# Performance work log

Measured on AMD Instinct MI355X. Metric: run time of the kernel, lower is better.

The kernel has to match this reference:

```python
import jax, jax.numpy as jnp
import numpy as np

NUM_GROUPS = 8
EPS = 1e-5
QB = 128.0  # 2 ** (8 - 1), b = 8 activation bits


def setup_inputs() -> dict:
    key = jax.random.key(0)
    k1, k2, k3 = jax.random.split(key, 3)
    B, IN, OUT = 8192, 4096, 4096
    x = jax.random.normal(k1, (B, IN), jnp.float32)
    # emulates the int8 sign buffer (values in {-1, +1}) stored as float
    qw = jnp.sign(jax.random.normal(k2, (OUT, IN), jnp.float32))
    bias = jax.random.normal(k3, (OUT,), jnp.float32) * 0.02
    return {"x": x, "qw": qw, "bias": bias}


def _ste_sign(z):
    # straight-through estimator: sign in fwd, identity grad in bwd
    return jax.lax.stop_gradient(jnp.sign(z) - z) + z


def reference(x, qw, bias):
    g = NUM_GROUPS
    # dequantize_weights: global mean-abs scale over the sign buffer
    alpha = jnp.mean(jnp.abs(qw))
    w = qw * alpha                                  # [OUT, IN]
    OUT, IN = w.shape
    # binarize_weights_groupwise: groups along out_features rows
    wg = w.reshape(g, OUT // g, IN)
    alpha_g = jnp.mean(jnp.abs(wg), axis=(1, 2), keepdims=True)
    bw = _ste_sign(wg - alpha_g).reshape(OUT, IN)   # values in {-1, 0, +1}
    # linear
    out = x @ bw.T + bias                           # [B, OUT]
    # quantize_activations_groupwise: groups along batch dim, b=8
    B = out.shape[0]
    og = out.reshape(g, B // g, OUT)
    gamma_g = jnp.max(jnp.abs(og), axis=(1, 2), keepdims=True)
    q = jnp.clip(og * QB / (gamma_g + EPS), -QB + EPS, QB - EPS)
    return q.reshape(B, OUT)
```

## Files before the change

### kernel.cpp

```cpp
#include <hip/hip_runtime.h>
#include <hip/hip_bf16.h>
#include <stdint.h>

#define B_DIM   8192
#define IN_DIM  4096
#define OUT_DIM 4096
#define QB_V    128.0f
#define EPS_V   1e-5f

typedef __attribute__((ext_vector_type(4))) float  f32x4;
typedef __attribute__((ext_vector_type(8))) __bf16 bf16x8;
typedef __attribute__((ext_vector_type(4))) __bf16 bf16x4;

__device__ __forceinline__ void gload_lds16(const void* g, void* l) {
  void* gp = const_cast<void*>(g);
  __builtin_amdgcn_global_load_lds(
      (__attribute__((address_space(1))) void*)gp,
      (__attribute__((address_space(3))) void*)l, 16, 0, 0);
}

__device__ __forceinline__ __bf16 sgnb(float d) {
  return (__bf16)((d > 0.f) ? 1.f : (d < 0.f ? -1.f : 0.f));
}

__global__ void k_init(unsigned* ws) {
  int t = threadIdx.x;
  if (t < 16) ws[t] = 0u;
}

__global__ __launch_bounds__(256) void k_qw_sums(const float* __restrict__ qw,
                                                 float* __restrict__ sums) {
  __shared__ float red[4];
  const int t = threadIdx.x;
  const size_t base = (size_t)blockIdx.x * 4096;
  float s = 0.f;
#pragma unroll
  for (int j = 0; j < 4; ++j) {
    f32x4 v = *(const f32x4*)(qw + base + (size_t)j * 1024 + t * 4);
    s += fabsf(v.x) + fabsf(v.y) + fabsf(v.z) + fabsf(v.w);
  }
#pragma unroll
  for (int off = 32; off > 0; off >>= 1) s += __shfl_xor(s, off);
  if ((t & 63) == 0) red[t >> 6] = s;
  __syncthreads();
  if (t == 0) {
    float bs = red[0] + red[1] + red[2] + red[3];
    atomicAdd(sums + (blockIdx.x >> 9), bs);
  }
}

__global__ __launch_bounds__(256) void k_conv_bw(const float* __restrict__ qw,
                                                 const float* __restrict__ sums,
                                                 __bf16* __restrict__ bw) {
  const size_t i = ((size_t)blockIdx.x * 256 + threadIdx.x) * 16;
  const int g = (int)(i >> 21);
  const float mu = sums[g] * (1.0f / 2097152.0f);
#pragma unroll
  for (int h = 0; h < 2; ++h) {
    f32x4 v0 = *(const f32x4*)(qw + i + h * 8);
    f32x4 v1 = *(const f32x4*)(qw + i + h * 8 + 4);
    bf16x8 r;
    r[0] = sgnb(v0.x - mu); r[1] = sgnb(v0.y - mu);
    r[2] = sgnb(v0.z - mu); r[3] = sgnb(v0.w - mu);
    r[4] = sgnb(v1.x - mu); r[5] = sgnb(v1.y - mu);
    r[6] = sgnb(v1.z - mu); r[7] = sgnb(v1.w - mu);
    *(bf16x8*)(bw + i + h * 8) = r;
  }
}

__global__ __launch_bounds__(256) void k_conv_x(const float* __restrict__ x,
                                                __bf16* __restrict__ xb) {
  const size_t i = ((size_t)blockIdx.x * 256 + threadIdx.x) * 16;
#pragma unroll
  for (int h = 0; h < 2; ++h) {
    f32x4 v0 = *(const f32x4*)(x + i + h * 8);
    f32x4 v1 = *(const f32x4*)(x + i + h * 8 + 4);
    bf16x8 r;
    r[0] = (__bf16)v0.x; r[1] = (__bf16)v0.y;
    r[2] = (__bf16)v0.z; r[3] = (__bf16)v0.w;
    r[4] = (__bf16)v1.x; r[5] = (__bf16)v1.y;
    r[6] = (__bf16)v1.z; r[7] = (__bf16)v1.w;
    *(bf16x8*)(xb + i + h * 8) = r;
  }
}

template <int AMODE>
__global__ __launch_bounds__(256) void k_gemm(
    const __bf16* __restrict__ xa, const float* __restrict__ xf,
    const __bf16* __restrict__ bwb, const float* __restrict__ qw,
    const float* __restrict__ sums, const float* __restrict__ bias,
    float* __restrict__ out, unsigned* __restrict__ gamma_bits) {
  __shared__ __bf16 As[128 * 64];
  __shared__ __bf16 Bs[128 * 64];
  const int t = threadIdx.x;
  const int lane = t & 63;
  const int wv = t >> 6;
  const int wr = wv >> 1, wc = wv & 1;
  const int fr = lane & 15, fq = lane >> 4;
  const int fr7 = fr & 7;
  const int orig = blockIdx.x;
  const int bid = ((orig & 7) << 8) | (orig >> 3);
  const int bm = bid & 63, bn = bid >> 6;
  const int brow = bm << 7, bcol = bn << 7;

  f32x4 acc[4][4] = {};

  const int c0row = t >> 3;
  const int cchunk = t & 7;
  const int schunk = cchunk ^ (c0row & 7);
  const int ccol = cchunk << 3;
  const int scol = schunk << 3;

  float muB = 0.f;
  if (AMODE == 2) muB = sums[bcol >> 9] * (1.0f / 2097152.0f);

  for (int kt = 0; kt < IN_DIM / 64; ++kt) {
    const int k0 = kt << 6;
    if (AMODE == 0) {
      __syncthreads();
#pragma unroll
      for (int it = 0; it < 4; ++it) {
        const int row = c0row + it * 32;
        gload_lds16(xa + (size_t)(brow + row) * IN_DIM + k0 + scol,
                    As + (row << 6) + ccol);
        gload_lds16(bwb + (size_t)(bcol + row) * IN_DIM + k0 + scol,
                    Bs + (row << 6) + ccol);
      }
      __syncthreads();
    } else if (AMODE == 1) {
      f32x4 a0[4], a1[4];
#pragma unroll
      for (int it = 0; it < 4; ++it) {
        const int row = c0row + it * 32;
        const float* p = xf + (size_t)(brow + row) * IN_DIM + k0 + scol;
        a0[it] = *(const f32x4*)p;
        a1[it] = *(const f32x4*)(p + 4);
      }
      __syncthreads();
#pragma unroll
      for (int it = 0; it < 4; ++it) {
        const int row = c0row + it * 32;
        gload_lds16(bwb + (size_t)(bcol + row) * IN_DIM + k0 + scol,
                    Bs + (row << 6) + ccol);
      }
#pragma unroll
      for (int it = 0; it < 4; ++it) {
        const int row = c0row + it * 32;
        bf16x8 w;
        w[0] = (__bf16)a0[it].x; w[1] = (__bf16)a0[it].y;
        w[2] = (__bf16)a0[it].z; w[3] = (__bf16)a0[it].w;
        w[4] = (__bf16)a1[it].x; w[5] = (__bf16)a1[it].y;
        w[6] = (__bf16)a1[it].z; w[7] = (__bf16)a1[it].w;
        *(bf16x8*)(As + (row << 6) + ccol) = w;
      }
      __syncthreads();
    } else {
      f32x4 a0[4], a1[4], b0[4], b1[4];
#pragma unroll
      for (int it = 0; it < 4; ++it) {
        const int row = c0row + it * 32;
        const float* pa = xf + (size_t)(brow + row) * IN_DIM + k0 + scol;
        a0[it] = *(const f32x4*)pa;
        a1[it] = *(const f32x4*)(pa + 4);
        const float* pb = qw + (size_t)(bcol + row) * IN_DIM + k0 + scol;
        b0[it] = *(const f32x4*)pb;
        b1[it] = *(const f32x4*)(pb + 4);
      }
      __syncthreads();
#pragma unroll
      for (int it = 0; it < 4; ++it) {
        const int row = c0row + it * 32;
        bf16x8 wa, wb;
        wa[0] = (__bf16)a0[it].x; wa[1] = (__bf16)a0[it].y;
        wa[2] = (__bf16)a0[it].z; wa[3] = (__bf16)a0[it].w;
        wa[4] = (__bf16)a1[it].x; wa[5] = (__bf16)a1[it].y;
        wa[6] = (__bf16)a1[it].z; wa[7] = (__bf16)a1[it].w;
        wb[0] = sgnb(b0[it].x - muB); wb[1] = sgnb(b0[it].y - muB);
        wb[2] = sgnb(b0[it].z - muB); wb[3] = sgnb(b0[it].w - muB);
        wb[4] = sgnb(b1[it].x - muB); wb[5] = sgnb(b1[it].y - muB);
        wb[6] = sgnb(b1[it].z - muB); wb[7] = sgnb(b1[it].w - muB);
        *(bf16x8*)(As + (row << 6) + ccol) = wa;
        *(bf16x8*)(Bs + (row << 6) + ccol) = wb;
      }
      __syncthreads();
    }

#pragma unroll
    for (int ks = 0; ks < 2; ++ks) {
      bf16x8 af[4], bfr[4];
#pragma unroll
      for (int mi = 0; mi < 4; ++mi)
        af[mi] = *(const bf16x8*)(As + (((wr << 6) + (mi << 4) + fr) << 6) +
                                  ((((ks << 2) | fq) ^ fr7) << 3));
#pragma unroll
      for (int ni = 0; ni < 4; ++ni)
        bfr[ni] = *(const bf16x8*)(Bs + (((wc << 6) + (ni << 4) + fr) << 6) +
                                   ((((ks << 2) | fq) ^ fr7) << 3));
#pragma unroll
      for (int mi = 0; mi < 4; ++mi)
#pragma unroll
        for (int ni = 0; ni < 4; ++ni)
          acc[mi][ni] = __builtin_amdgcn_mfma_f32_16x16x32_bf16(
              af[mi], bfr[ni], acc[mi][ni], 0, 0, 0);
    }
  }

  float mx = 0.f;
  const int colbase = bcol + (wc << 6);
#pragma unroll
  for (int ni = 0; ni < 4; ++ni) {
    const int col = colbase + (ni << 4) + fr;
    const float bv = bias[col];
#pragma unroll
    for (int mi = 0; mi < 4; ++mi) {
      const int rowb = brow + (wr << 6) + (mi << 4) + (fq << 2);
#pragma unroll
      for (int j = 0; j < 4; ++j) {
        const float v = acc[mi][ni][j] + bv;
        out[(size_t)(rowb + j) * OUT_DIM + col] = v;
        mx = fmaxf(mx, fabsf(v));
      }
    }
  }
#pragma unroll
  for (int off = 32; off > 0; off >>= 1) mx = fmaxf(mx, __shfl_xor(mx, off));
  if (lane == 0)
    atomicMax(gamma_bits + (brow >> 10), __float_as_uint(mx));
}

__global__ __launch_bounds__(256) void k_scale(float* __restrict__ out,
                                               const unsigned* __restrict__ gb) {
  const size_t i = ((size_t)blockIdx.x * 256 + threadIdx.x) * 16;
  const int g = (int)(i >> 22);
  const float gamma = __uint_as_float(gb[g]);
  const float sc = QB_V / (gamma + EPS_V);
  const float lo = -QB_V + EPS_V, hi = QB_V - EPS_V;
#pragma unroll
  for (int h = 0; h < 4; ++h) {
    f32x4 v = *(const f32x4*)(out + i + h * 4);
    v.x = fminf(fmaxf(v.x * sc, lo), hi);
    v.y = fminf(fmaxf(v.y * sc, lo), hi);
    v.z = fminf(fmaxf(v.z * sc, lo), hi);
    v.w = fminf(fmaxf(v.w * sc, lo), hi);
    *(f32x4*)(out + i + h * 4) = v;
  }
}

extern "C" void kernel_launch(void* const* d_in, const int* in_sizes, int n_in,
                              void* d_out, int out_size, void* d_ws,
                              size_t ws_size, hipStream_t stream) {
  const float* x = (const float*)d_in[0];
  const float* qw = (const float*)d_in[1];
  const float* bias = (const float*)d_in[2];
  float* out = (float*)d_out;
  char* ws = (char*)d_ws;
  float* sums = (float*)ws;
  unsigned* gamma = (unsigned*)ws + 8;
  __bf16* bwb = (__bf16*)(ws + 256);
  __bf16* xb = (__bf16*)(ws + 256 + (size_t)OUT_DIM * IN_DIM * 2);

  const size_t need1 = 256 + (size_t)OUT_DIM * IN_DIM * 2;
  const size_t need0 = need1 + (size_t)B_DIM * IN_DIM * 2;
  const int amode = (ws_size >= need0) ? 0 : ((ws_size >= need1) ? 1 : 2);

  k_init<<<1, 64, 0, stream>>>((unsigned*)ws);
  k_qw_sums<<<4096, 256, 0, stream>>>(qw, sums);
  if (amode <= 1) k_conv_bw<<<4096, 256, 0, stream>>>(qw, sums, bwb);
  if (amode == 0) k_conv_x<<<8192, 256, 0, stream>>>(x, xb);

  if (amode == 0)
    k_gemm<0><<<2048, 256, 0, stream>>>(xb, x, bwb, qw, sums, bias, out, gamma);
  else if (amode == 1)
    k_gemm<1><<<2048, 256, 0, stream>>>(xb, x, bwb, qw, sums, bias, out, gamma);
  else
    k_gemm<2><<<2048, 256, 0, stream>>>(xb, x, bwb, qw, sums, bias, out, gamma);

  k_scale<<<8192, 256, 0, stream>>>(out, gamma);
}
```

Baseline: 819.5 us.

## Rewrite GEMM with 256x256 double-buffered tiles and fuse conversion kernels

Replaces the 128x128 single-buffered GEMM with a 256x256 tile, 512-thread kernel. It double-buffers LDS, prefetches the next k-tile with direct global-to-LDS loads and manual vmcnt waits, and raises MFMA priority with s_setprio. It also merges the weight and activation bf16 conversion kernels into one grid-stride kernel and makes the sums and scale kernels grid-stride. The fallback modes for small workspace are removed. The larger tile increases reuse per load, but uses 128KB of LDS and many accumulator registers, which may limit occupancy to one block per CU.

New measurement: 701.2 us. 14.4% less time.

```diff
diff --git a/kernel.cpp b/kernel.cpp
--- a/kernel.cpp
+++ b/kernel.cpp
@@ -10,7 +10,6 @@
 
 typedef __attribute__((ext_vector_type(4))) float  f32x4;
 typedef __attribute__((ext_vector_type(8))) __bf16 bf16x8;
-typedef __attribute__((ext_vector_type(4))) __bf16 bf16x4;
 
 __device__ __forceinline__ void gload_lds16(const void* g, void* l) {
   void* gp = const_cast<void*>(g);
@@ -32,191 +31,158 @@
                                                  float* __restrict__ sums) {
   __shared__ float red[4];
   const int t = threadIdx.x;
-  const size_t base = (size_t)blockIdx.x * 4096;
-  float s = 0.f;
-#pragma unroll
-  for (int j = 0; j < 4; ++j) {
-    f32x4 v = *(const f32x4*)(qw + base + (size_t)j * 1024 + t * 4);
-    s += fabsf(v.x) + fabsf(v.y) + fabsf(v.z) + fabsf(v.w);
-  }
-#pragma unroll
-  for (int off = 32; off > 0; off >>= 1) s += __shfl_xor(s, off);
-  if ((t & 63) == 0) red[t >> 6] = s;
-  __syncthreads();
-  if (t == 0) {
-    float bs = red[0] + red[1] + red[2] + red[3];
-    atomicAdd(sums + (blockIdx.x >> 9), bs);
-  }
-}
-
-__global__ __launch_bounds__(256) void k_conv_bw(const float* __restrict__ qw,
-                                                 const float* __restrict__ sums,
-                                                 __bf16* __restrict__ bw) {
-  const size_t i = ((size_t)blockIdx.x * 256 + threadIdx.x) * 16;
-  const int g = (int)(i >> 21);
-  const float mu = sums[g] * (1.0f / 2097152.0f);
-#pragma unroll
-  for (int h = 0; h < 2; ++h) {
-    f32x4 v0 = *(const f32x4*)(qw + i + h * 8);
-    f32x4 v1 = *(const f32x4*)(qw + i + h * 8 + 4);
-    bf16x8 r;
-    r[0] = sgnb(v0.x - mu); r[1] = sgnb(v0.y - mu);
-    r[2] = sgnb(v0.z - mu); r[3] = sgnb(v0.w - mu);
-    r[4] = sgnb(v1.x - mu); r[5] = sgnb(v1.y - mu);
-    r[6] = sgnb(v1.z - mu); r[7] = sgnb(v1.w - mu);
-    *(bf16x8*)(bw + i + h * 8) = r;
-  }
-}
-
-__global__ __launch_bounds__(256) void k_conv_x(const float* __restrict__ x,
-                                                __bf16* __restrict__ xb) {
-  const size_t i = ((size_t)blockIdx.x * 256 + threadIdx.x) * 16;
-#pragma unroll
-  for (int h = 0; h < 2; ++h) {
-    f32x4 v0 = *(const f32x4*)(x + i + h * 8);
-    f32x4 v1 = *(const f32x4*)(x + i + h * 8 + 4);
-    bf16x8 r;
-    r[0] = (__bf16)v0.x; r[1] = (__bf16)v0.y;
-    r[2] = (__bf16)v0.z; r[3] = (__bf16)v0.w;
-    r[4] = (__bf16)v1.x; r[5] = (__bf16)v1.y;
-    r[6] = (__bf16)v1.z; r[7] = (__bf16)v1.w;
-    *(bf16x8*)(xb + i + h * 8) = r;
-  }
-}
-
-template <int AMODE>
-__global__ __launch_bounds__(256) void k_gemm(
-    const __bf16* __restrict__ xa, const float* __restrict__ xf,
-    const __bf16* __restrict__ bwb, const float* __restrict__ qw,
-    const float* __restrict__ sums, const float* __restrict__ bias,
-    float* __restrict__ out, unsigned* __restrict__ gamma_bits) {
-  __shared__ __bf16 As[128 * 64];
-  __shared__ __bf16 Bs[128 * 64];
+  for (int vb = blockIdx.x; vb < 4096; vb += 2048) {
+    const size_t base = (size_t)vb * 4096;
+    float s = 0.f;
+#pragma unroll
+    for (int j = 0; j < 4; ++j) {
+      f32x4 v = *(const f32x4*)(qw + base + (size_t)j * 1024 + t * 4);
+      s += fabsf(v.x) + fabsf(v.y) + fabsf(v.z) + fabsf(v.w);
+    }
+#pragma unroll
+    for (int off = 32; off > 0; off >>= 1) s += __shfl_xor(s, off);
+    __syncthreads();
+    if ((t & 63) == 0) red[t >> 6] = s;
+    __syncthreads();
+    if (t == 0)
+      atomicAdd(sums + (vb >> 9), red[0] + red[1] + red[2] + red[3]);
+  }
+}
+
+__global__ __launch_bounds__(256) void k_conv(const float* __restrict__ qw,
+                                              const float* __restrict__ sums,
+                                              __bf16* __restrict__ bw,
+                                              const float* __restrict__ x,
+                                              __bf16* __restrict__ xb) {
+  const int t = threadIdx.x;
+  for (int vb = blockIdx.x; vb < 12288; vb += 2048) {
+    if (vb < 4096) {
+      const size_t i = ((size_t)vb * 256 + t) * 16;
+      const float mu = sums[(int)(i >> 21)] * (1.0f / 2097152.0f);
+#pragma unroll
+      for (int h = 0; h < 2; ++h) {
+        f32x4 v0 = *(const f32x4*)(qw + i + h * 8);
+        f32x4 v1 = *(const f32x4*)(qw + i + h * 8 + 4);
+        bf16x8 r;
+        r[0] = sgnb(v0.x - mu); r[1] = sgnb(v0.y - mu);
+        r[2] = sgnb(v0.z - mu); r[3] = sgnb(v0.w - mu);
+        r[4] = sgnb(v1.x - mu); r[5] = sgnb(v1.y - mu);
+        r[6] = sgnb(v1.z - mu); r[7] = sgnb(v1.w - mu);
+        *(bf16x8*)(bw + i + h * 8) = r;
+      }
+    } else {
+      const size_t i = ((size_t)(vb - 4096) * 256 + t) * 16;
+#pragma unroll
+      for (int h = 0; h < 2; ++h) {
+        f32x4 v0 = *(const f32x4*)(x + i + h * 8);
+        f32x4 v1 = *(const f32x4*)(x + i + h * 8 + 4);
+        bf16x8 r;
+        r[0] = (__bf16)v0.x; r[1] = (__bf16)v0.y;
+        r[2] = (__bf16)v0.z; r[3] = (__bf16)v0.w;
+        r[4] = (__bf16)v1.x; r[5] = (__bf16)v1.y;
+        r[6] = (__bf16)v1.z; r[7] = (__bf16)v1.w;
+        *(bf16x8*)(xb + i + h * 8) = r;
+      }
+    }
+  }
+}
+
+__global__ __launch_bounds__(512, 2) void k_gemm256(
+    const __bf16* __restrict__ xa, const __bf16* __restrict__ bwb,
+    const float* __restrict__ bias, float* __restrict__ out,
+    unsigned* __restrict__ gamma_bits) {
+  __shared__ __bf16 As[2][256 * 64];
+  __shared__ __bf16 Bs[2][256 * 64];
   const int t = threadIdx.x;
   const int lane = t & 63;
   const int wv = t >> 6;
-  const int wr = wv >> 1, wc = wv & 1;
+  const int wr = wv >> 2;
+  const int wc = wv & 3;
   const int fr = lane & 15, fq = lane >> 4;
   const int fr7 = fr & 7;
+
   const int orig = blockIdx.x;
-  const int bid = ((orig & 7) << 8) | (orig >> 3);
-  const int bm = bid & 63, bn = bid >> 6;
-  const int brow = bm << 7, bcol = bn << 7;
-
-  f32x4 acc[4][4] = {};
-
-  const int c0row = t >> 3;
+  const int bid = ((orig & 7) << 6) | (orig >> 3);
+  const int bm = bid & 31, bn = bid >> 5;
+  const int brow = bm << 8, bcol = bn << 8;
+
+  const int srow = t >> 3;
   const int cchunk = t & 7;
-  const int schunk = cchunk ^ (c0row & 7);
-  const int ccol = cchunk << 3;
-  const int scol = schunk << 3;
-
-  float muB = 0.f;
-  if (AMODE == 2) muB = sums[bcol >> 9] * (1.0f / 2097152.0f);
-
-  for (int kt = 0; kt < IN_DIM / 64; ++kt) {
-    const int k0 = kt << 6;
-    if (AMODE == 0) {
-      __syncthreads();
-#pragma unroll
-      for (int it = 0; it < 4; ++it) {
-        const int row = c0row + it * 32;
-        gload_lds16(xa + (size_t)(brow + row) * IN_DIM + k0 + scol,
-                    As + (row << 6) + ccol);
-        gload_lds16(bwb + (size_t)(bcol + row) * IN_DIM + k0 + scol,
-                    Bs + (row << 6) + ccol);
-      }
-      __syncthreads();
-    } else if (AMODE == 1) {
-      f32x4 a0[4], a1[4];
-#pragma unroll
-      for (int it = 0; it < 4; ++it) {
-        const int row = c0row + it * 32;
-        const float* p = xf + (size_t)(brow + row) * IN_DIM + k0 + scol;
-        a0[it] = *(const f32x4*)p;
-        a1[it] = *(const f32x4*)(p + 4);
-      }
-      __syncthreads();
-#pragma unroll
-      for (int it = 0; it < 4; ++it) {
-        const int row = c0row + it * 32;
-        gload_lds16(bwb + (size_t)(bcol + row) * IN_DIM + k0 + scol,
-                    Bs + (row << 6) + ccol);
-      }
-#pragma unroll
-      for (int it = 0; it < 4; ++it) {
-        const int row = c0row + it * 32;
-        bf16x8 w;
-        w[0] = (__bf16)a0[it].x; w[1] = (__bf16)a0[it].y;
-        w[2] = (__bf16)a0[it].z; w[3] = (__bf16)a0[it].w;
-        w[4] = (__bf16)a1[it].x; w[5] = (__bf16)a1[it].y;
-        w[6] = (__bf16)a1[it].z; w[7] = (__bf16)a1[it].w;
-        *(bf16x8*)(As + (row << 6) + ccol) = w;
-      }
-      __syncthreads();
+  const int schunk = cchunk ^ (srow & 7);
+  const int dstoff = (srow << 6) + (cchunk << 3);
+  const __bf16* aRow = xa + (size_t)(brow + srow) * IN_DIM + (schunk << 3);
+  const __bf16* bRow = bwb + (size_t)(bcol + srow) * IN_DIM + (schunk << 3);
+
+#define STAGE_A(kt, dd)                                                     \
+  {                                                                         \
+    const int _k0 = (kt) << 6;                                              \
+    _Pragma("unroll") for (int r = 0; r < 4; ++r)                           \
+        gload_lds16(aRow + (size_t)(r << 6) * IN_DIM + _k0,                 \
+                    &As[dd][(r << 12) + dstoff]);                           \
+  }
+#define STAGE_B(kt, dd)                                                     \
+  {                                                                         \
+    const int _k0 = (kt) << 6;                                              \
+    _Pragma("unroll") for (int r = 0; r < 4; ++r)                           \
+        gload_lds16(bRow + (size_t)(r << 6) * IN_DIM + _k0,                 \
+                    &Bs[dd][(r << 12) + dstoff]);                           \
+  }
+
+  f32x4 acc[8][4] = {};
+
+  STAGE_A(0, 0);
+  STAGE_B(0, 0);
+
+  int d = 0;
+  for (int kt = 0; kt < 64; ++kt) {
+    __builtin_amdgcn_s_barrier();
+    if (kt < 63) {
+      STAGE_A(kt + 1, d ^ 1);
+      asm volatile("s_waitcnt vmcnt(4)" ::: "memory");
     } else {
-      f32x4 a0[4], a1[4], b0[4], b1[4];
-#pragma unroll
-      for (int it = 0; it < 4; ++it) {
-        const int row = c0row + it * 32;
-        const float* pa = xf + (size_t)(brow + row) * IN_DIM + k0 + scol;
-        a0[it] = *(const f32x4*)pa;
-        a1[it] = *(const f32x4*)(pa + 4);
-        const float* pb = qw + (size_t)(bcol + row) * IN_DIM + k0 + scol;
-        b0[it] = *(const f32x4*)pb;
-        b1[it] = *(const f32x4*)(pb + 4);
-      }
-      __syncthreads();
-#pragma unroll
-      for (int it = 0; it < 4; ++it) {
-        const int row = c0row + it * 32;
-        bf16x8 wa, wb;
-        wa[0] = (__bf16)a0[it].x; wa[1] = (__bf16)a0[it].y;
-        wa[2] = (__bf16)a0[it].z; wa[3] = (__bf16)a0[it].w;
-        wa[4] = (__bf16)a1[it].x; wa[5] = (__bf16)a1[it].y;
-        wa[6] = (__bf16)a1[it].z; wa[7] = (__bf16)a1[it].w;
-        wb[0] = sgnb(b0[it].x - muB); wb[1] = sgnb(b0[it].y - muB);
-        wb[2] = sgnb(b0[it].z - muB); wb[3] = sgnb(b0[it].w - muB);
-        wb[4] = sgnb(b1[it].x - muB); wb[5] = sgnb(b1[it].y - muB);
-        wb[6] = sgnb(b1[it].z - muB); wb[7] = sgnb(b1[it].w - muB);
-        *(bf16x8*)(As + (row << 6) + ccol) = wa;
-        *(bf16x8*)(Bs + (row << 6) + ccol) = wb;
-      }
-      __syncthreads();
-    }
+      asm volatile("s_waitcnt vmcnt(0)" ::: "memory");
+    }
+    __builtin_amdgcn_s_barrier();
 
 #pragma unroll
     for (int ks = 0; ks < 2; ++ks) {
-      bf16x8 af[4], bfr[4];
-#pragma unroll
-      for (int mi = 0; mi < 4; ++mi)
-        af[mi] = *(const bf16x8*)(As + (((wr << 6) + (mi << 4) + fr) << 6) +
-                                  ((((ks << 2) | fq) ^ fr7) << 3));
-#pragma unroll
-      for (int ni = 0; ni < 4; ++ni)
-        bfr[ni] = *(const bf16x8*)(Bs + (((wc << 6) + (ni << 4) + fr) << 6) +
-                                   ((((ks << 2) | fq) ^ fr7) << 3));
-#pragma unroll
-      for (int mi = 0; mi < 4; ++mi)
-#pragma unroll
-        for (int ni = 0; ni < 4; ++ni)
-          acc[mi][ni] = __builtin_amdgcn_mfma_f32_16x16x32_bf16(
-              af[mi], bfr[ni], acc[mi][ni], 0, 0, 0);
-    }
-  }
+      const int cs = (ks << 2) | fq;
+      bf16x8 af[8], bfv[4];
+#pragma unroll
+      for (int m = 0; m < 8; ++m)
+        af[m] = *(const bf16x8*)(&As[d][(((wr << 7) + (m << 4) + fr) << 6) +
+                                        ((cs ^ fr7) << 3)]);
+#pragma unroll
+      for (int n = 0; n < 4; ++n)
+        bfv[n] = *(const bf16x8*)(&Bs[d][(((wc << 6) + (n << 4) + fr) << 6) +
+                                         ((cs ^ fr7) << 3)]);
+      __builtin_amdgcn_s_setprio(1);
+#pragma unroll
+      for (int m = 0; m < 8; ++m)
+#pragma unroll
+        for (int n = 0; n < 4; ++n)
+          acc[m][n] = __builtin_amdgcn_mfma_f32_16x16x32_bf16(
+              af[m], bfv[n], acc[m][n], 0, 0, 0);
+      __builtin_amdgcn_s_setprio(0);
+      if (ks == 0 && kt < 63) STAGE_B(kt + 1, d ^ 1);
+    }
+    d ^= 1;
+  }
+#undef STAGE_A
+#undef STAGE_B
 
   float mx = 0.f;
   const int colbase = bcol + (wc << 6);
 #pragma unroll
-  for (int ni = 0; ni < 4; ++ni) {
-    const int col = colbase + (ni << 4) + fr;
+  for (int n = 0; n < 4; ++n) {
+    const int col = colbase + (n << 4) + fr;
     const float bv = bias[col];
 #pragma unroll
-    for (int mi = 0; mi < 4; ++mi) {
-      const int rowb = brow + (wr << 6) + (mi << 4) + (fq << 2);
+    for (int m = 0; m < 8; ++m) {
+      const int rowb = brow + (wr << 7) + (m << 4) + (fq << 2);
 #pragma unroll
       for (int j = 0; j < 4; ++j) {
-        const float v = acc[mi][ni][j] + bv;
+        const float v = acc[m][n][j] + bv;
         out[(size_t)(rowb + j) * OUT_DIM + col] = v;
         mx = fmaxf(mx, fabsf(v));
       }
@@ -230,19 +196,21 @@
 
 __global__ __launch_bounds__(256) void k_scale(float* __restrict__ out,
                                                const unsigned* __restrict__ gb) {
-  const size_t i = ((size_t)blockIdx.x * 256 + threadIdx.x) * 16;
-  const int g = (int)(i >> 22);
-  const float gamma = __uint_as_float(gb[g]);
-  const float sc = QB_V / (gamma + EPS_V);
-  const float lo = -QB_V + EPS_V, hi = QB_V - EPS_V;
-#pragma unroll
-  for (int h = 0; h < 4; ++h) {
-    f32x4 v = *(const f32x4*)(out + i + h * 4);
-    v.x = fminf(fmaxf(v.x * sc, lo), hi);
-    v.y = fminf(fmaxf(v.y * sc, lo), hi);
-    v.z = fminf(fmaxf(v.z * sc, lo), hi);
-    v.w = fminf(fmaxf(v.w * sc, lo), hi);
-    *(f32x4*)(out + i + h * 4) = v;
+  const int t = threadIdx.x;
+  for (int vb = blockIdx.x; vb < 8192; vb += 2048) {
+    const size_t i = ((size_t)vb * 256 + t) * 16;
+    const float gamma = __uint_as_float(gb[(int)(i >> 22)]);
+    const float sc = QB_V / (gamma + EPS_V);
+    const float lo = -QB_V + EPS_V, hi = QB_V - EPS_V;
+#pragma unroll
+    for (int h = 0; h < 4; ++h) {
+      f32x4 v = *(const f32x4*)(out + i + h * 4);
+      v.x = fminf(fmaxf(v.x * sc, lo), hi);
+      v.y = fminf(fmaxf(v.y * sc, lo), hi);
+      v.z = fminf(fmaxf(v.z * sc, lo), hi);
+      v.w = fminf(fmaxf(v.w * sc, lo), hi);
+      *(f32x4*)(out + i + h * 4) = v;
+    }
   }
 }
 
@@ -259,21 +227,9 @@
   __bf16* bwb = (__bf16*)(ws + 256);
   __bf16* xb = (__bf16*)(ws + 256 + (size_t)OUT_DIM * IN_DIM * 2);
 
-  const size_t need1 = 256 + (size_t)OUT_DIM * IN_DIM * 2;
-  const size_t need0 = need1 + (size_t)B_DIM * IN_DIM * 2;
-  const int amode = (ws_size >= need0) ? 0 : ((ws_size >= need1) ? 1 : 2);
-
   k_init<<<1, 64, 0, stream>>>((unsigned*)ws);
-  k_qw_sums<<<4096, 256, 0, stream>>>(qw, sums);
-  if (amode <= 1) k_conv_bw<<<4096, 256, 0, stream>>>(qw, sums, bwb);
-  if (amode == 0) k_conv_x<<<8192, 256, 0, stream>>>(x, xb);
-
-  if (amode == 0)
-    k_gemm<0><<<2048, 256, 0, stream>>>(xb, x, bwb, qw, sums, bias, out, gamma);
-  else if (amode == 1)
-    k_gemm<1><<<2048, 256, 0, stream>>>(xb, x, bwb, qw, sums, bias, out, gamma);
-  else
-    k_gemm<2><<<2048, 256, 0, stream>>>(xb, x, bwb, qw, sums, bias, out, gamma);
-
-  k_scale<<<8192, 256, 0, stream>>>(out, gamma);
-}
+  k_qw_sums<<<2048, 256, 0, stream>>>(qw, sums);
+  k_conv<<<2048, 256, 0, stream>>>(qw, sums, bwb, x, xb);
+  k_gemm256<<<512, 512, 0, stream>>>(xb, bwb, bias, out, gamma);
+  k_scale<<<2048, 256, 0, stream>>>(out, gamma);
+}
```
